# Kernel optimization log

Hardware: AMD Instinct MI355X
Metric: run time of the kernel (lower is better)

The kernel has to match this reference:

```python
import jax, jax.numpy as jnp
import numpy as np

CORR_THRESHOLD = 0.5
EPS = 1e-12


def setup_inputs() -> dict:
    key = jax.random.key(0)
    # x: [B, N_channels, T] EEG windows
    x = jax.random.normal(key, (128, 64, 30720), dtype=jnp.float32)
    return {"x": x}


def reference(x):
    # Batched Pearson correlation across channels (rows = variables, like np.corrcoef).
    B, N, T = x.shape
    xc = x - jnp.mean(x, axis=-1, keepdims=True)            # center over time
    cov = jnp.einsum("bnt,bmt->bnm", xc, xc)                # [B, N, N] unnormalized
    norms = jnp.sqrt(jnp.einsum("bnt,bnt->bn", xc, xc))     # [B, N] row L2 norms
    corr = cov / (norms[:, :, None] * norms[:, None, :] + EPS)
    # zero diagonal, then threshold on |corr|
    eye = jnp.eye(N, dtype=bool)
    corr = jnp.where(eye[None], 0.0, corr)
    mask = jnp.abs(corr) >= CORR_THRESHOLD
    adj = jnp.where(mask, corr, 0.0)                        # dense masked adjacency [B, N, N]
    # node features are the raw EEG samples (as in the original Data(x=eeg_sample, ...))
    return adj, x
```

## Files before the change

### kernel.cpp

```cpp
#include <hip/hip_runtime.h>
#include <hip/hip_bf16.h>
#include <cstdint>
#include <cstddef>

#define B_   128
#define NCH  64
#define T_   30720
#define EPSF 1e-12f
#define THRF 0.5f

typedef float  f32x4 __attribute__((ext_vector_type(4)));
typedef short  s16x8 __attribute__((ext_vector_type(8)));
typedef unsigned short u16;

#define AS1 __attribute__((address_space(1)))
#define AS3 __attribute__((address_space(3)))

static __device__ __forceinline__ short bf16s(float f) {
    return (short)__builtin_bit_cast(u16, __float2bfloat16(f));
}

__global__ __launch_bounds__(256) void corr_stage1(
    const float* __restrict__ x, float* __restrict__ out_x,
    float* __restrict__ P, float* __restrict__ S,
    int split, int Tc)
{
    __shared__ __align__(16) float lds[2][NCH * 128];

    const int tid  = threadIdx.x;
    const int lane = tid & 63;
    const int w    = tid >> 6;

    const int bid = blockIdx.x;
    const int b   = bid / split;
    const int c   = bid - b * split;

    const size_t base = (size_t)b * ((size_t)NCH * T_) + (size_t)c * Tc;
    const float* xw = x + base;
    float*       ow = out_x + base;

    const int NT = Tc >> 7;

    const int sg = lane & 31;
    const int hi = lane >> 5;

    const int fr = lane & 15;
    const int g8 = lane >> 4;
    const int fs = fr & 7;

    f32x4 acc[4];
    #pragma unroll
    for (int cb = 0; cb < 4; ++cb) acc[cb] = (f32x4)(0.f);
    float csum[8];
    #pragma unroll
    for (int kk = 0; kk < 8; ++kk) csum[kk] = 0.f;

    auto dma = [&](int tile, int buf) {
        #pragma unroll
        for (int kk = 0; kk < 8; ++kk) {
            const int k  = w * 8 + kk;
            const int ch = 2 * k + hi;
            const int gg = sg ^ (ch & 7);
            const float* src = xw + (size_t)ch * T_ + (size_t)(tile * 128 + gg * 4);
            float* dst = &lds[buf][k * 256];
            __builtin_amdgcn_global_load_lds((const AS1 void*)src,
                                             (AS3 void*)dst, 16, 0, 0);
        }
    };

    dma(0, 0);
    asm volatile("s_waitcnt vmcnt(0)" ::: "memory");
    __builtin_amdgcn_s_barrier();
    __builtin_amdgcn_sched_barrier(0);

    for (int t = 0; t < NT; ++t) {
        const int cur = t & 1;
        if (t + 1 < NT) dma(t + 1, cur ^ 1);

        #pragma unroll
        for (int kk = 0; kk < 8; ++kk) {
            const int k   = w * 8 + kk;
            const int row = 2 * k + hi;
            const f32x4 v = *reinterpret_cast<const f32x4*>(
                &lds[cur][row * 128 + ((sg ^ (row & 7)) << 2)]);
            float* q = ow + (size_t)row * T_ + (size_t)(t * 128 + sg * 4);
            *reinterpret_cast<f32x4*>(q) = v;
            csum[kk] += ((v.x + v.y) + (v.z + v.w));
        }

        #pragma unroll
        for (int ks = 0; ks < 4; ++ks) {
            const int g0 = ks * 8 + g8 * 2;
            const f32x4 alo = *reinterpret_cast<const f32x4*>(
                &lds[cur][(w * 16 + fr) * 128 + ((g0 ^ fs) << 2)]);
            const f32x4 ahi = *reinterpret_cast<const f32x4*>(
                &lds[cur][(w * 16 + fr) * 128 + (((g0 + 1) ^ fs) << 2)]);
            s16x8 Af;
            Af[0] = bf16s(alo.x); Af[1] = bf16s(alo.y);
            Af[2] = bf16s(alo.z); Af[3] = bf16s(alo.w);
            Af[4] = bf16s(ahi.x); Af[5] = bf16s(ahi.y);
            Af[6] = bf16s(ahi.z); Af[7] = bf16s(ahi.w);
            #pragma unroll
            for (int cb = 0; cb < 4; ++cb) {
                s16x8 Bf;
                if (cb == w) {
                    Bf = Af;
                } else {
                    const f32x4 blo = *reinterpret_cast<const f32x4*>(
                        &lds[cur][(cb * 16 + fr) * 128 + ((g0 ^ fs) << 2)]);
                    const f32x4 bhi = *reinterpret_cast<const f32x4*>(
                        &lds[cur][(cb * 16 + fr) * 128 + (((g0 + 1) ^ fs) << 2)]);
                    Bf[0] = bf16s(blo.x); Bf[1] = bf16s(blo.y);
                    Bf[2] = bf16s(blo.z); Bf[3] = bf16s(blo.w);
                    Bf[4] = bf16s(bhi.x); Bf[5] = bf16s(bhi.y);
                    Bf[6] = bf16s(bhi.z); Bf[7] = bf16s(bhi.w);
                }
                acc[cb] = __builtin_amdgcn_mfma_f32_16x16x32_bf16(Af, Bf, acc[cb], 0, 0, 0);
            }
        }

        asm volatile("s_waitcnt vmcnt(8)" ::: "memory");
        __builtin_amdgcn_s_barrier();
        __builtin_amdgcn_sched_barrier(0);
    }

    #pragma unroll
    for (int kk = 0; kk < 8; ++kk) {
        float v = csum[kk];
        v += __shfl_xor(v, 1,  64);
        v += __shfl_xor(v, 2,  64);
        v += __shfl_xor(v, 4,  64);
        v += __shfl_xor(v, 8,  64);
        v += __shfl_xor(v, 16, 64);
        if ((lane & 31) == 0) {
            const int row = 2 * (w * 8 + kk) + hi;
            S[(size_t)bid * NCH + row] = v;
        }
    }

    float* Pc = P + ((size_t)bid << 12);
    const int prow = (lane >> 4) << 2;
    const int pcol = lane & 15;
    #pragma unroll
    for (int cb = 0; cb < 4; ++cb)
        #pragma unroll
        for (int reg = 0; reg < 4; ++reg)
            Pc[(w * 16 + prow + reg) * 64 + cb * 16 + pcol] = acc[cb][reg];
}

__global__ __launch_bounds__(256) void corr_stage2(
    const float* __restrict__ P, const float* __restrict__ S,
    float* __restrict__ adj, int split)
{
    const int idx = blockIdx.x * 256 + threadIdx.x;
    const int b  = idx >> 12;
    const int nm = idx & 4095;
    const int n  = nm >> 6;
    const int m  = nm & 63;

    float G = 0.f, Gnn = 0.f, Gmm = 0.f, Sn = 0.f, Sm = 0.f;
    for (int c = 0; c < split; ++c) {
        const float* Pc = P + ((size_t)(b * split + c) << 12);
        const float* Sc = S + (size_t)(b * split + c) * NCH;
        G   += Pc[nm];
        Gnn += Pc[n * 65];
        Gmm += Pc[m * 65];
        Sn  += Sc[n];
        Sm  += Sc[m];
    }
    const float invT = 1.0f / (float)T_;
    const float cov  = G   - Sn * Sm * invT;
    const float vn   = Gnn - Sn * Sn * invT;
    const float vm   = Gmm - Sm * Sm * invT;
    const float den  = sqrtf(vn) * sqrtf(vm) + EPSF;
    float corr = cov / den;
    if (n == m) corr = 0.f;
    adj[idx] = (fabsf(corr) >= THRF) ? corr : 0.f;
}

extern "C" void kernel_launch(void* const* d_in, const int* in_sizes, int n_in,
                              void* d_out, int out_size, void* d_ws, size_t ws_size,
                              hipStream_t stream)
{
    const float* x   = (const float*)d_in[0];
    float* out   = (float*)d_out;
    float* adj   = out;
    float* out_x = out + (size_t)B_ * NCH * NCH;

    int split = 4;
    while (split > 1 &&
           (size_t)B_ * split * (4096 + NCH) * sizeof(float) > ws_size)
        split >>= 1;

    float* P = (float*)d_ws;
    float* S = P + (size_t)B_ * split * 4096;
    const int Tc = T_ / split;

    corr_stage1<<<dim3(B_ * split), dim3(256), 0, stream>>>(x, out_x, P, S, split, Tc);
    corr_stage2<<<dim3((B_ * 4096) / 256), dim3(256), 0, stream>>>(P, S, adj, split);
}
```

Before: 443.5 us.

## Specialize warps: four copy/sum the tile, four compute Gram via MFMA

Stage 1 now launches 512 threads per block and splits the waves into two roles. Four waves copy each LDS tile to the output x and accumulate row sums. The other four waves each compute a 32x32 quadrant of the Gram matrix with 2x2 MFMA register tiles. All eight waves share the DMA of each tile into LDS, with four loads per wave instead of eight. The aim is to overlap the store-bound copy with the MFMA work inside one block, at the cost of larger blocks and extra barrier coupling between the two roles.

```diff
diff --git a/kernel.cpp b/kernel.cpp
--- a/kernel.cpp
+++ b/kernel.cpp
@@ -20,7 +20,7 @@
     return (short)__builtin_bit_cast(u16, __float2bfloat16(f));
 }
 
-__global__ __launch_bounds__(256) void corr_stage1(
+__global__ __launch_bounds__(512) void corr_stage1(
     const float* __restrict__ x, float* __restrict__ out_x,
     float* __restrict__ P, float* __restrict__ S,
     int split, int Tc)
@@ -41,28 +41,17 @@
 
     const int NT = Tc >> 7;
 
+    const int hi = lane >> 5;
     const int sg = lane & 31;
-    const int hi = lane >> 5;
-
-    const int fr = lane & 15;
-    const int g8 = lane >> 4;
-    const int fs = fr & 7;
-
-    f32x4 acc[4];
-    #pragma unroll
-    for (int cb = 0; cb < 4; ++cb) acc[cb] = (f32x4)(0.f);
-    float csum[8];
-    #pragma unroll
-    for (int kk = 0; kk < 8; ++kk) csum[kk] = 0.f;
 
     auto dma = [&](int tile, int buf) {
         #pragma unroll
-        for (int kk = 0; kk < 8; ++kk) {
-            const int k  = w * 8 + kk;
-            const int ch = 2 * k + hi;
+        for (int i = 0; i < 4; ++i) {
+            const int j  = w * 4 + i;
+            const int ch = 2 * j + hi;
             const int gg = sg ^ (ch & 7);
             const float* src = xw + (size_t)ch * T_ + (size_t)(tile * 128 + gg * 4);
-            float* dst = &lds[buf][k * 256];
+            float* dst = &lds[buf][j * 256];
             __builtin_amdgcn_global_load_lds((const AS1 void*)src,
                                              (AS3 void*)dst, 16, 0, 0);
         }
@@ -73,79 +62,101 @@
     __builtin_amdgcn_s_barrier();
     __builtin_amdgcn_sched_barrier(0);
 
-    for (int t = 0; t < NT; ++t) {
-        const int cur = t & 1;
-        if (t + 1 < NT) dma(t + 1, cur ^ 1);
+    if (w < 4) {
+        float csum[8];
+        #pragma unroll
+        for (int kk = 0; kk < 8; ++kk) csum[kk] = 0.f;
+
+        for (int t = 0; t < NT; ++t) {
+            const int cur = t & 1;
+            if (t + 1 < NT) dma(t + 1, cur ^ 1);
+
+            #pragma unroll
+            for (int kk = 0; kk < 8; ++kk) {
+                const int row = 16 * w + 2 * kk + hi;
+                const f32x4 v = *reinterpret_cast<const f32x4*>(
+                    &lds[cur][row * 128 + ((sg ^ (row & 7)) << 2)]);
+                *reinterpret_cast<f32x4*>(
+                    ow + (size_t)row * T_ + (size_t)(t * 128 + sg * 4)) = v;
+                csum[kk] += ((v.x + v.y) + (v.z + v.w));
+            }
+
+            asm volatile("s_waitcnt vmcnt(8)" ::: "memory");
+            __builtin_amdgcn_s_barrier();
+            __builtin_amdgcn_sched_barrier(0);
+        }
 
         #pragma unroll
         for (int kk = 0; kk < 8; ++kk) {
-            const int k   = w * 8 + kk;
-            const int row = 2 * k + hi;
-            const f32x4 v = *reinterpret_cast<const f32x4*>(
-                &lds[cur][row * 128 + ((sg ^ (row & 7)) << 2)]);
-            float* q = ow + (size_t)row * T_ + (size_t)(t * 128 + sg * 4);
-            *reinterpret_cast<f32x4*>(q) = v;
-            csum[kk] += ((v.x + v.y) + (v.z + v.w));
-        }
-
-        #pragma unroll
-        for (int ks = 0; ks < 4; ++ks) {
-            const int g0 = ks * 8 + g8 * 2;
-            const f32x4 alo = *reinterpret_cast<const f32x4*>(
-                &lds[cur][(w * 16 + fr) * 128 + ((g0 ^ fs) << 2)]);
-            const f32x4 ahi = *reinterpret_cast<const f32x4*>(
-                &lds[cur][(w * 16 + fr) * 128 + (((g0 + 1) ^ fs) << 2)]);
-            s16x8 Af;
-            Af[0] = bf16s(alo.x); Af[1] = bf16s(alo.y);
-            Af[2] = bf16s(alo.z); Af[3] = bf16s(alo.w);
-            Af[4] = bf16s(ahi.x); Af[5] = bf16s(ahi.y);
-            Af[6] = bf16s(ahi.z); Af[7] = bf16s(ahi.w);
-            #pragma unroll
-            for (int cb = 0; cb < 4; ++cb) {
-                s16x8 Bf;
-                if (cb == w) {
-                    Bf = Af;
-                } else {
-                    const f32x4 blo = *reinterpret_cast<const f32x4*>(
-                        &lds[cur][(cb * 16 + fr) * 128 + ((g0 ^ fs) << 2)]);
-                    const f32x4 bhi = *reinterpret_cast<const f32x4*>(
-                        &lds[cur][(cb * 16 + fr) * 128 + (((g0 + 1) ^ fs) << 2)]);
-                    Bf[0] = bf16s(blo.x); Bf[1] = bf16s(blo.y);
-                    Bf[2] = bf16s(blo.z); Bf[3] = bf16s(blo.w);
-                    Bf[4] = bf16s(bhi.x); Bf[5] = bf16s(bhi.y);
-                    Bf[6] = bf16s(bhi.z); Bf[7] = bf16s(bhi.w);
+            float v = csum[kk];
+            v += __shfl_xor(v, 1,  64);
+            v += __shfl_xor(v, 2,  64);
+            v += __shfl_xor(v, 4,  64);
+            v += __shfl_xor(v, 8,  64);
+            v += __shfl_xor(v, 16, 64);
+            if ((lane & 31) == 0)
+                S[(size_t)bid * NCH + 16 * w + 2 * kk + hi] = v;
+        }
+    } else {
+        const int q  = w - 4;
+        const int qr = q >> 1, qc = q & 1;
+        const int fr = lane & 15;
+        const int g8 = lane >> 4;
+        const int fs = fr & 7;
+
+        f32x4 acc[2][2];
+        #pragma unroll
+        for (int rb = 0; rb < 2; ++rb)
+            #pragma unroll
+            for (int cb = 0; cb < 2; ++cb) acc[rb][cb] = (f32x4)(0.f);
+
+        for (int t = 0; t < NT; ++t) {
+            const int cur = t & 1;
+            if (t + 1 < NT) dma(t + 1, cur ^ 1);
+
+            #pragma unroll
+            for (int ks = 0; ks < 4; ++ks) {
+                const int gl = (ks * 8 + 2 * g8) ^ fs;
+                const int gh = (ks * 8 + 2 * g8 + 1) ^ fs;
+                s16x8 frag[4];
+                #pragma unroll
+                for (int e = 0; e < 4; ++e) {
+                    const int blk = (e < 2) ? (2 * qr + e) : (2 * qc + (e - 2));
+                    const int ro  = (blk * 16 + fr) * 128;
+                    const f32x4 lo = *reinterpret_cast<const f32x4*>(
+                        &lds[cur][ro + (gl << 2)]);
+                    const f32x4 hv = *reinterpret_cast<const f32x4*>(
+                        &lds[cur][ro + (gh << 2)]);
+                    frag[e][0] = bf16s(lo.x); frag[e][1] = bf16s(lo.y);
+                    frag[e][2] = bf16s(lo.z); frag[e][3] = bf16s(lo.w);
+                    frag[e][4] = bf16s(hv.x); frag[e][5] = bf16s(hv.y);
+                    frag[e][6] = bf16s(hv.z); frag[e][7] = bf16s(hv.w);
                 }
-                acc[cb] = __builtin_amdgcn_mfma_f32_16x16x32_bf16(Af, Bf, acc[cb], 0, 0, 0);
+                #pragma unroll
+                for (int rb = 0; rb < 2; ++rb)
+                    #pragma unroll
+                    for (int cb = 0; cb < 2; ++cb)
+                        acc[rb][cb] = __builtin_amdgcn_mfma_f32_16x16x32_bf16(
+                            frag[rb], frag[2 + cb], acc[rb][cb], 0, 0, 0);
             }
-        }
-
-        asm volatile("s_waitcnt vmcnt(8)" ::: "memory");
-        __builtin_amdgcn_s_barrier();
-        __builtin_amdgcn_sched_barrier(0);
+
+            asm volatile("s_waitcnt vmcnt(0)" ::: "memory");
+            __builtin_amdgcn_s_barrier();
+            __builtin_amdgcn_sched_barrier(0);
+        }
+
+        float* Pc = P + ((size_t)bid << 12);
+        const int prow = (lane >> 4) << 2;
+        const int pcol = lane & 15;
+        #pragma unroll
+        for (int rb = 0; rb < 2; ++rb)
+            #pragma unroll
+            for (int cb = 0; cb < 2; ++cb)
+                #pragma unroll
+                for (int reg = 0; reg < 4; ++reg)
+                    Pc[((2 * qr + rb) * 16 + prow + reg) * 64
+                       + (2 * qc + cb) * 16 + pcol] = acc[rb][cb][reg];
     }
-
-    #pragma unroll
-    for (int kk = 0; kk < 8; ++kk) {
-        float v = csum[kk];
-        v += __shfl_xor(v, 1,  64);
-        v += __shfl_xor(v, 2,  64);
-        v += __shfl_xor(v, 4,  64);
-        v += __shfl_xor(v, 8,  64);
-        v += __shfl_xor(v, 16, 64);
-        if ((lane & 31) == 0) {
-            const int row = 2 * (w * 8 + kk) + hi;
-            S[(size_t)bid * NCH + row] = v;
-        }
-    }
-
-    float* Pc = P + ((size_t)bid << 12);
-    const int prow = (lane >> 4) << 2;
-    const int pcol = lane & 15;
-    #pragma unroll
-    for (int cb = 0; cb < 4; ++cb)
-        #pragma unroll
-        for (int reg = 0; reg < 4; ++reg)
-            Pc[(w * 16 + prow + reg) * 64 + cb * 16 + pcol] = acc[cb][reg];
 }
 
 __global__ __launch_bounds__(256) void corr_stage2(
@@ -196,6 +207,6 @@
     float* S = P + (size_t)B_ * split * 4096;
     const int Tc = T_ / split;
 
-    corr_stage1<<<dim3(B_ * split), dim3(256), 0, stream>>>(x, out_x, P, S, split, Tc);
+    corr_stage1<<<dim3(B_ * split), dim3(512), 0, stream>>>(x, out_x, P, S, split, Tc);
     corr_stage2<<<dim3((B_ * 4096) / 256), dim3(256), 0, stream>>>(P, S, adj, split);
 }
```

Result: faster. 433.2 us (-2.3%).
